# Optimization experiments

Measured on AMD Instinct MI355X. Metric: run time of the kernel, lower is better.

The kernel has to match this reference:

```python
import jax, jax.numpy as jnp
import numpy as np

B, Q, K = 8, 128, 1024
QK_DIM = 512   # query_size == key_size
HID = 256      # hidden_size
VDIM = 512     # value feature dim
NEG = -1e6     # mask fill value used by the torch code


def setup_inputs() -> dict:
    key = jax.random.key(0)
    ks = jax.random.split(key, 7)
    queries = jax.random.normal(ks[0], (B, Q, QK_DIM), dtype=jnp.float32)
    keys = jax.random.normal(ks[1], (B, K, QK_DIM), dtype=jnp.float32)
    values = jax.random.normal(ks[2], (B, K, VDIM), dtype=jnp.float32)
    valid_lens = jax.random.randint(ks[3], (B,), 1, K + 1, dtype=jnp.int32)
    # Linear weights (no bias); scaled like torch default init
    Wq = jax.random.normal(ks[4], (QK_DIM, HID), dtype=jnp.float32) / np.sqrt(QK_DIM)
    Wk = jax.random.normal(ks[5], (QK_DIM, HID), dtype=jnp.float32) / np.sqrt(QK_DIM)
    wv = jax.random.normal(ks[6], (HID,), dtype=jnp.float32) / np.sqrt(HID)
    return {"queries": queries, "keys": keys, "values": values,
            "valid_lens": valid_lens, "Wq": Wq, "Wk": Wk, "wv": wv}


def reference(queries, keys, values, valid_lens, Wq, Wk, wv):
    q = jnp.einsum('bqd,dh->bqh', queries, Wq)          # [B,Q,H]
    k = jnp.einsum('bkd,dh->bkh', keys, Wk)             # [B,K,H]
    # broadcast add -> tanh -> score projection
    features = jnp.tanh(q[:, :, None, :] + k[:, None, :, :])  # [B,Q,K,H]
    scores = jnp.einsum('bqkh,h->bqk', features, wv)    # [B,Q,K]
    # masked softmax over last axis (valid_lens per batch row)
    mask = jnp.arange(scores.shape[-1])[None, None, :] < valid_lens[:, None, None]
    scores = jnp.where(mask, scores, NEG)
    attn = jax.nn.softmax(scores, axis=-1)              # [B,Q,K]
    # dropout is identity in eval mode (p=0)
    return jnp.einsum('bqk,bkv->bqv', attn, values)     # [B,Q,VDIM]
```

## Files before the change

### kernel.cpp

```cpp
#include <hip/hip_runtime.h>
#include <math.h>

#define NB 8
#define NQ 128
#define NK 1024
#define ND 512
#define NH 256
#define NV 512

typedef __attribute__((ext_vector_type(8))) short short8v;
typedef __attribute__((ext_vector_type(4))) float floatx4;

__device__ __forceinline__ ushort f2bf(float f) {
  union { float f; unsigned u; } v; v.f = f;
  unsigned r = (v.u + 0x7FFF + ((v.u >> 16) & 1)) >> 16;
  return (ushort)r;
}
__device__ __forceinline__ float bf2f(ushort b) {
  union { unsigned u; float f; } v; v.u = ((unsigned)b) << 16;
  return v.f;
}
__device__ __forceinline__ float wave_rsum(float v) {
#pragma unroll
  for (int off = 32; off; off >>= 1) v += __shfl_xor(v, off);
  return v;
}

__global__ __launch_bounds__(256) void splitw_kernel(
    const float* __restrict__ Wq, const float* __restrict__ Wk,
    ushort* __restrict__ WtQh, ushort* __restrict__ WtQl,
    ushort* __restrict__ WtKh, ushort* __restrict__ WtKl) {
  const int t = threadIdx.x;
  const int mat = blockIdx.x >> 7;
  const int bi = blockIdx.x & 127;
  const int d0 = (bi >> 3) * 32, h0 = (bi & 7) * 32;
  const float* W = mat ? Wk : Wq;
  ushort* Oh = mat ? WtKh : WtQh;
  ushort* Ol = mat ? WtKl : WtQl;
  __shared__ float tile[32][33];
#pragma unroll
  for (int i = 0; i < 4; ++i) {
    int idx = t + 256 * i;
    int r = idx >> 5, c = idx & 31;
    tile[r][c] = W[(size_t)(d0 + r) * NH + h0 + c];
  }
  __syncthreads();
#pragma unroll
  for (int i = 0; i < 4; ++i) {
    int idx = t + 256 * i;
    int hh = idx >> 5, dd = idx & 31;
    float f = tile[dd][hh];
    ushort hi = f2bf(f);
    float lo = f - bf2f(hi);
    Oh[(size_t)(h0 + hh) * ND + d0 + dd] = hi;
    Ol[(size_t)(h0 + hh) * ND + d0 + dd] = f2bf(lo);
  }
}

__global__ __launch_bounds__(256) void convert_v_kernel(
    const float* __restrict__ values, const int* __restrict__ valid_lens,
    ushort* __restrict__ VhT) {
  const int b = blockIdx.z;
  const int k0 = blockIdx.x * 32;
  const int v0 = blockIdx.y * 32;
  const int V = valid_lens[b];
  if (k0 >= ((V + 31) & ~31)) return;
  const int t = threadIdx.x;
  __shared__ float tile[32][33];
#pragma unroll
  for (int i = 0; i < 4; ++i) {
    int idx = t + 256 * i;
    int kk = idx >> 5, vv = idx & 31;
    tile[kk][vv] = values[(size_t)(b * NK + k0 + kk) * NV + v0 + vv];
  }
  __syncthreads();
#pragma unroll
  for (int i = 0; i < 4; ++i) {
    int idx = t + 256 * i;
    int vv = idx >> 5, kk = idx & 31;
    VhT[(size_t)(b * NV + v0 + vv) * NK + k0 + kk] = f2bf(tile[kk][vv]);
  }
}

__global__ __launch_bounds__(256) void proj_mfma_kernel(
    const float* __restrict__ queries, const float* __restrict__ keys,
    const ushort* __restrict__ WtQh, const ushort* __restrict__ WtQl,
    const ushort* __restrict__ WtKh, const ushort* __restrict__ WtKl,
    const int* __restrict__ valid_lens,
    float* __restrict__ Eq, ushort* __restrict__ EkTb) {
  const int t = threadIdx.x;
  const int lane = t & 63, wvid = t >> 6;
  const int lr = lane & 15, lg = lane >> 4;
  const int bx = blockIdx.x;
  const bool isQ = bx < 64;
  const float* A;
  const ushort *Wh, *Wl;
  int arow0, b = 0, rin = 0;
  if (isQ) {
    A = queries; Wh = WtQh; Wl = WtQl; arow0 = bx * 16;
  } else {
    int kt = bx - 64;
    b = kt >> 6; rin = (kt & 63) * 16;
    if (rin >= valid_lens[b]) return;
    A = keys; Wh = WtKh; Wl = WtKl; arow0 = b * NK + rin;
  }

  __shared__ ushort Ah[16][520];
  __shared__ ushort Al[16][520];
  {
    const float* Arow = A + (size_t)arow0 * ND;
#pragma unroll
    for (int i = 0; i < 8; ++i) {
      int e = (t + 256 * i) * 4;
      int r = e >> 9, c = e & 511;
      float4 a = *(const float4*)&Arow[e];
      ushort4 h, l;
      h.x = f2bf(a.x); l.x = f2bf(a.x - bf2f(h.x));
      h.y = f2bf(a.y); l.y = f2bf(a.y - bf2f(h.y));
      h.z = f2bf(a.z); l.z = f2bf(a.z - bf2f(h.z));
      h.w = f2bf(a.w); l.w = f2bf(a.w - bf2f(h.w));
      *(ushort4*)&Ah[r][c] = h;
      *(ushort4*)&Al[r][c] = l;
    }
  }
  __syncthreads();

  const int c0w = wvid * 64;
  const ushort* Whb = Wh + (size_t)(c0w + lr) * ND + lg * 8;
  const ushort* Wlb = Wl + (size_t)(c0w + lr) * ND + lg * 8;

  floatx4 acc[4];
#pragma unroll
  for (int cf = 0; cf < 4; ++cf) acc[cf] = (floatx4){0.f, 0.f, 0.f, 0.f};

#define LOADW(dsth, dstl, kkv)                                            \
  {                                                                       \
    const size_t _d = (size_t)(kkv) * 32;                                 \
    dsth##0 = *(const short8v*)&Whb[_d];                                  \
    dstl##0 = *(const short8v*)&Wlb[_d];                                  \
    dsth##1 = *(const short8v*)&Whb[(size_t)16 * ND + _d];                \
    dstl##1 = *(const short8v*)&Wlb[(size_t)16 * ND + _d];                \
    dsth##2 = *(const short8v*)&Whb[(size_t)32 * ND + _d];                \
    dstl##2 = *(const short8v*)&Wlb[(size_t)32 * ND + _d];                \
    dsth##3 = *(const short8v*)&Whb[(size_t)48 * ND + _d];                \
    dstl##3 = *(const short8v*)&Wlb[(size_t)48 * ND + _d];                \
  }

#define MFMA4(ah_, al_, wh, wl)                                           \
  {                                                                       \
    acc[0] = __builtin_amdgcn_mfma_f32_16x16x32_bf16(al_, wh##0, acc[0], 0, 0, 0); \
    acc[0] = __builtin_amdgcn_mfma_f32_16x16x32_bf16(ah_, wl##0, acc[0], 0, 0, 0); \
    acc[0] = __builtin_amdgcn_mfma_f32_16x16x32_bf16(ah_, wh##0, acc[0], 0, 0, 0); \
    acc[1] = __builtin_amdgcn_mfma_f32_16x16x32_bf16(al_, wh##1, acc[1], 0, 0, 0); \
    acc[1] = __builtin_amdgcn_mfma_f32_16x16x32_bf16(ah_, wl##1, acc[1], 0, 0, 0); \
    acc[1] = __builtin_amdgcn_mfma_f32_16x16x32_bf16(ah_, wh##1, acc[1], 0, 0, 0); \
    acc[2] = __builtin_amdgcn_mfma_f32_16x16x32_bf16(al_, wh##2, acc[2], 0, 0, 0); \
    acc[2] = __builtin_amdgcn_mfma_f32_16x16x32_bf16(ah_, wl##2, acc[2], 0, 0, 0); \
    acc[2] = __builtin_amdgcn_mfma_f32_16x16x32_bf16(ah_, wh##2, acc[2], 0, 0, 0); \
    acc[3] = __builtin_amdgcn_mfma_f32_16x16x32_bf16(al_, wh##3, acc[3], 0, 0, 0); \
    acc[3] = __builtin_amdgcn_mfma_f32_16x16x32_bf16(ah_, wl##3, acc[3], 0, 0, 0); \
    acc[3] = __builtin_amdgcn_mfma_f32_16x16x32_bf16(ah_, wh##3, acc[3], 0, 0, 0); \
  }

  short8v wAh0, wAh1, wAh2, wAh3, wAl0, wAl1, wAl2, wAl3;
  short8v wBh0, wBh1, wBh2, wBh3, wBl0, wBl1, wBl2, wBl3;
  LOADW(wAh, wAl, 0);
#pragma unroll 1
  for (int kk = 0; kk < 16; kk += 2) {
    LOADW(wBh, wBl, kk + 1);
    {
      short8v ah_ = *(const short8v*)&Ah[lr][kk * 32 + lg * 8];
      short8v al_ = *(const short8v*)&Al[lr][kk * 32 + lg * 8];
      MFMA4(ah_, al_, wAh, wAl);
    }
    if (kk + 2 < 16) LOADW(wAh, wAl, kk + 2);
    {
      short8v ah_ = *(const short8v*)&Ah[lr][(kk + 1) * 32 + lg * 8];
      short8v al_ = *(const short8v*)&Al[lr][(kk + 1) * 32 + lg * 8];
      MFMA4(ah_, al_, wBh, wBl);
    }
  }
#undef LOADW
#undef MFMA4

  const float C2 = 2.885390081777927f;
  if (isQ) {
#pragma unroll
    for (int cf = 0; cf < 4; ++cf) {
      const int h = c0w + cf * 16 + lr;
#pragma unroll
      for (int reg = 0; reg < 4; ++reg) {
        const int row = arow0 + lg * 4 + reg;
        float p = fminf(fmaxf(acc[cf][reg], -15.f), 15.f);
        Eq[(size_t)row * NH + h] = exp2f(p * C2);
      }
    }
  } else {
#pragma unroll
    for (int cf = 0; cf < 4; ++cf) {
      const int h = c0w + cf * 16 + lr;
      ushort4 e;
      e.x = f2bf(exp2f(fminf(fmaxf(acc[cf][0], -15.f), 15.f) * C2));
      e.y = f2bf(exp2f(fminf(fmaxf(acc[cf][1], -15.f), 15.f) * C2));
      e.z = f2bf(exp2f(fminf(fmaxf(acc[cf][2], -15.f), 15.f) * C2));
      e.w = f2bf(exp2f(fminf(fmaxf(acc[cf][3], -15.f), 15.f) * C2));
      *(ushort4*)&EkTb[((size_t)(b * NH + h)) * NK + rin + lg * 4] = e;
    }
  }
}

__global__ __launch_bounds__(256) void score_kernel(
    const float* __restrict__ Eq, const ushort* __restrict__ EkTb,
    const float* __restrict__ wvp, const int* __restrict__ valid_lens,
    ushort* __restrict__ Pb, float* __restrict__ rowsum) {
  const int b = blockIdx.z;
  const int V = valid_lens[b];
  const int k0 = blockIdx.y * 256;
  if (k0 >= V) return;
  const int t = threadIdx.x;
  const int q0 = blockIdx.x * 2;
  const int lane = t & 63, wid = t >> 6;
  const float L2E2 = 2.8853900817779268f;

  __shared__ __align__(16) float eqs[2][NH];
  __shared__ __align__(16) float wvs[NH];
  __shared__ float red[8];

  if (t < 128)
    ((float4*)eqs)[t] = ((const float4*)&Eq[(size_t)(b * NQ + q0) * NH])[t];
  wvs[t] = wvp[t];
  __syncthreads();

  float mn = wave_rsum(fminf(wvs[t], 0.f));
  if (lane == 0) red[wid] = mn;
  __syncthreads();
  const float SN = -(red[0] + red[1] + red[2] + red[3]);
  __syncthreads();

  const ushort* ek = EkTb + (size_t)b * NH * NK + k0 + t;
  float acc0 = 0.f, acc1 = 0.f;

  ushort uA[8], uB[8];
#define LOADE(u, h0)                                                      \
  {                                                                       \
    _Pragma("unroll") for (int j = 0; j < 8; ++j)                         \
        u[j] = ek[(size_t)((h0) + j) * NK];                               \
  }
#define CHUNK(u, h0)                                                      \
  {                                                                       \
    float e0[8], e1[8], w8[8];                                            \
    *(float4*)&e0[0] = *(const float4*)&eqs[0][(h0)];                     \
    *(float4*)&e0[4] = *(const float4*)&eqs[0][(h0) + 4];                 \
    *(float4*)&e1[0] = *(const float4*)&eqs[1][(h0)];                     \
    *(float4*)&e1[4] = *(const float4*)&eqs[1][(h0) + 4];                 \
    *(float4*)&w8[0] = *(const float4*)&wvs[(h0)];                        \
    *(float4*)&w8[4] = *(const float4*)&wvs[(h0) + 4];                    \
    _Pragma("unroll") for (int j = 0; j < 8; ++j) {                       \
      const float ev = bf2f(u[j]);                                        \
      acc0 += w8[j] * __builtin_amdgcn_rcpf(__builtin_fmaf(e0[j], ev, 1.f)); \
      acc1 += w8[j] * __builtin_amdgcn_rcpf(__builtin_fmaf(e1[j], ev, 1.f)); \
    }                                                                     \
  }

  LOADE(uA, 0);
#pragma unroll 1
  for (int h0 = 0; h0 < NH; h0 += 16) {
    LOADE(uB, h0 + 8);
    CHUNK(uA, h0);
    if (h0 + 16 < NH) LOADE(uA, h0 + 16);
    CHUNK(uB, h0 + 8);
  }
#undef LOADE
#undef CHUNK

  const int k = k0 + t;
  const float p0 = (k < V) ? exp2f(-L2E2 * (acc0 + SN)) : 0.f;
  const float p1 = (k < V) ? exp2f(-L2E2 * (acc1 + SN)) : 0.f;
  const ushort u0 = f2bf(p0), u1 = f2bf(p1);
  Pb[(size_t)(b * NQ + q0) * NK + k] = u0;
  Pb[(size_t)(b * NQ + q0 + 1) * NK + k] = u1;

  float s0 = wave_rsum(bf2f(u0));
  float s1 = wave_rsum(bf2f(u1));
  if (lane == 0) { red[wid] = s0; red[4 + wid] = s1; }
  __syncthreads();
  if (t == 0) {
    atomicAdd(&rowsum[b * NQ + q0], red[0] + red[1] + red[2] + red[3]);
    atomicAdd(&rowsum[b * NQ + q0 + 1], red[4] + red[5] + red[6] + red[7]);
  }
}

__global__ __launch_bounds__(128) void pv_mfma_kernel(
    const ushort* __restrict__ Pb, const ushort* __restrict__ VhT,
    const float* __restrict__ rowsum, const int* __restrict__ valid_lens,
    float* __restrict__ out) {
  const int w = threadIdx.x >> 6;
  const int lane = threadIdx.x & 63;
  const int lr = lane & 15, lg = lane >> 4;
  const int qt = blockIdx.x, vt = blockIdx.y, b = blockIdx.z;
  const int V = valid_lens[b];
  const int Kt = (V + 31) >> 5;
  const int q0 = qt * 16;
  const int v0 = vt * 32 + w * 16;
  const ushort* pp = Pb + (size_t)(b * NQ + q0 + lr) * NK + lg * 8;
  const ushort* vp = VhT + (size_t)(b * NV + v0 + lr) * NK + lg * 8;

  floatx4 accA = (floatx4){0.f, 0.f, 0.f, 0.f};
  floatx4 accB = (floatx4){0.f, 0.f, 0.f, 0.f};
  short8v pa, va, pb, vb;

  pa = *(const short8v*)&pp[0];
  va = *(const short8v*)&vp[0];
  if (Kt > 1) {
    pb = *(const short8v*)&pp[32];
    vb = *(const short8v*)&vp[32];
  }
  int s = 0;
  while (s + 2 <= Kt) {
    accA = __builtin_amdgcn_mfma_f32_16x16x32_bf16(pa, va, accA, 0, 0, 0);
    if (s + 2 < Kt) {
      pa = *(const short8v*)&pp[(size_t)(s + 2) * 32];
      va = *(const short8v*)&vp[(size_t)(s + 2) * 32];
    }
    accB = __builtin_amdgcn_mfma_f32_16x16x32_bf16(pb, vb, accB, 0, 0, 0);
    if (s + 3 < Kt) {
      pb = *(const short8v*)&pp[(size_t)(s + 3) * 32];
      vb = *(const short8v*)&vp[(size_t)(s + 3) * 32];
    }
    s += 2;
  }
  if (s < Kt)
    accA = __builtin_amdgcn_mfma_f32_16x16x32_bf16(pa, va, accA, 0, 0, 0);

#pragma unroll
  for (int reg = 0; reg < 4; ++reg) {
    const int row = b * NQ + q0 + lg * 4 + reg;
    const float rs = __builtin_amdgcn_rcpf(rowsum[row]);
    out[(size_t)row * NV + v0 + lr] = (accA[reg] + accB[reg]) * rs;
  }
}

extern "C" void kernel_launch(void* const* d_in, const int* in_sizes, int n_in,
                              void* d_out, int out_size, void* d_ws, size_t ws_size,
                              hipStream_t stream) {
  const float* queries = (const float*)d_in[0];
  const float* keys    = (const float*)d_in[1];
  const float* values  = (const float*)d_in[2];
  const int*   vlens   = (const int*)d_in[3];
  const float* Wq      = (const float*)d_in[4];
  const float* Wk      = (const float*)d_in[5];
  const float* wv      = (const float*)d_in[6];
  float* out = (float*)d_out;

  char* base = (char*)d_ws;
  ushort* WtQh = (ushort*)base;
  ushort* WtQl = WtQh + NH * ND;
  ushort* WtKh = WtQl + NH * ND;
  ushort* WtKl = WtKh + NH * ND;
  float*  Eq   = (float*)(base + (1 << 20));
  ushort* EkTb = (ushort*)(base + (2 << 20));
  ushort* Pb   = (ushort*)(base + (6 << 20));
  ushort* VhT  = (ushort*)(base + (8 << 20));
  float*  rowsum = (float*)(base + (16 << 20));

  hipMemsetAsync(rowsum, 0, NB * NQ * sizeof(float), stream);
  splitw_kernel<<<dim3(256), dim3(256), 0, stream>>>(Wq, Wk, WtQh, WtQl, WtKh, WtKl);
  convert_v_kernel<<<dim3(32, 16, 8), dim3(256), 0, stream>>>(values, vlens, VhT);
  proj_mfma_kernel<<<dim3(576), dim3(256), 0, stream>>>(
      queries, keys, WtQh, WtQl, WtKh, WtKl, vlens, Eq, EkTb);
  score_kernel<<<dim3(64, 4, 8), dim3(256), 0, stream>>>(
      Eq, EkTb, wv, vlens, Pb, rowsum);
  pv_mfma_kernel<<<dim3(8, 16, 8), dim3(128), 0, stream>>>(
      Pb, VhT, rowsum, vlens, out);
}
```

Baseline: 181.4 us.

## Pack W, V and P into MFMA fragment-order tiles for contiguous lane loads

The weight split, V conversion and score kernels now write their bf16 outputs in a tiled layout that matches the MFMA operand fragments. Each lane can then load a contiguous 16-byte chunk with a lane*8 stride instead of doing strided row gathers. The projection and PV kernels are rewritten to read these packed tiles, with deeper register prefetch (triple-buffered W, four-stage P/V) and launch-bounds occupancy hints. PV now rounds the K-tile count up to a multiple of 4. That can read V tiles the conversion kernel never wrote, so any non-finite leftovers in the workspace could reach the output.

```diff
diff --git a/kernel.cpp b/kernel.cpp
--- a/kernel.cpp
+++ b/kernel.cpp
@@ -11,6 +11,7 @@
 typedef __attribute__((ext_vector_type(8))) short short8v;
 typedef __attribute__((ext_vector_type(4))) float floatx4;
 
+
 __device__ __forceinline__ ushort f2bf(float f) {
   union { float f; unsigned u; } v; v.f = f;
   unsigned r = (v.u + 0x7FFF + ((v.u >> 16) & 1)) >> 16;
@@ -26,40 +27,33 @@
   return v;
 }
 
-__global__ __launch_bounds__(256) void splitw_kernel(
+__global__ __launch_bounds__(64) void splitw_kernel(
     const float* __restrict__ Wq, const float* __restrict__ Wk,
-    ushort* __restrict__ WtQh, ushort* __restrict__ WtQl,
-    ushort* __restrict__ WtKh, ushort* __restrict__ WtKl) {
-  const int t = threadIdx.x;
-  const int mat = blockIdx.x >> 7;
-  const int bi = blockIdx.x & 127;
-  const int d0 = (bi >> 3) * 32, h0 = (bi & 7) * 32;
-  const float* W = mat ? Wk : Wq;
-  ushort* Oh = mat ? WtKh : WtQh;
-  ushort* Ol = mat ? WtKl : WtQl;
-  __shared__ float tile[32][33];
-#pragma unroll
-  for (int i = 0; i < 4; ++i) {
-    int idx = t + 256 * i;
-    int r = idx >> 5, c = idx & 31;
-    tile[r][c] = W[(size_t)(d0 + r) * NH + h0 + c];
-  }
-  __syncthreads();
-#pragma unroll
-  for (int i = 0; i < 4; ++i) {
-    int idx = t + 256 * i;
-    int hh = idx >> 5, dd = idx & 31;
-    float f = tile[dd][hh];
+    ushort* __restrict__ WpQ, ushort* __restrict__ WpK) {
+  const int l = threadIdx.x;
+  const int blk = blockIdx.x;
+  const float* W = blockIdx.y ? Wk : Wq;
+  ushort* O = blockIdx.y ? WpK : WpQ;
+  const int col = ((blk >> 4) << 4) + (l & 15);
+  const int dbase = (blk & 15) * 32 + ((l >> 4) << 3);
+  ushort h8[8], l8[8];
+#pragma unroll
+  for (int j = 0; j < 8; ++j) {
+    float f = W[(size_t)(dbase + j) * NH + col];
     ushort hi = f2bf(f);
-    float lo = f - bf2f(hi);
-    Oh[(size_t)(h0 + hh) * ND + d0 + dd] = hi;
-    Ol[(size_t)(h0 + hh) * ND + d0 + dd] = f2bf(lo);
-  }
+    h8[j] = hi;
+    l8[j] = f2bf(f - bf2f(hi));
+  }
+  ushort* oh = &O[(size_t)blk * 1024 + l * 8];
+  *(ushort4*)&oh[0] = make_ushort4(h8[0], h8[1], h8[2], h8[3]);
+  *(ushort4*)&oh[4] = make_ushort4(h8[4], h8[5], h8[6], h8[7]);
+  *(ushort4*)&oh[512] = make_ushort4(l8[0], l8[1], l8[2], l8[3]);
+  *(ushort4*)&oh[516] = make_ushort4(l8[4], l8[5], l8[6], l8[7]);
 }
 
 __global__ __launch_bounds__(256) void convert_v_kernel(
     const float* __restrict__ values, const int* __restrict__ valid_lens,
-    ushort* __restrict__ VhT) {
+    ushort* __restrict__ Vp) {
   const int b = blockIdx.z;
   const int k0 = blockIdx.x * 32;
   const int v0 = blockIdx.y * 32;
@@ -74,18 +68,21 @@
     tile[kk][vv] = values[(size_t)(b * NK + k0 + kk) * NV + v0 + vv];
   }
   __syncthreads();
-#pragma unroll
-  for (int i = 0; i < 4; ++i) {
-    int idx = t + 256 * i;
-    int vv = idx >> 5, kk = idx & 31;
-    VhT[(size_t)(b * NV + v0 + vv) * NK + k0 + kk] = f2bf(tile[kk][vv]);
-  }
-}
-
-__global__ __launch_bounds__(256) void proj_mfma_kernel(
+  const int vv = t & 31, k4 = t >> 5;
+  const int kr = k4 * 4;
+  const size_t base = ((size_t)(b * 32 + ((v0 + vv) >> 4)) * 32 + (k0 >> 5)) * 512;
+  const int off = ((vv & 15) << 3) + (((kr >> 3) & 3) << 7) + (kr & 7);
+  ushort4 o;
+  o.x = f2bf(tile[kr + 0][vv]);
+  o.y = f2bf(tile[kr + 1][vv]);
+  o.z = f2bf(tile[kr + 2][vv]);
+  o.w = f2bf(tile[kr + 3][vv]);
+  *(ushort4*)&Vp[base + off] = o;
+}
+
+__global__ __launch_bounds__(256, 2) void proj_mfma_kernel(
     const float* __restrict__ queries, const float* __restrict__ keys,
-    const ushort* __restrict__ WtQh, const ushort* __restrict__ WtQl,
-    const ushort* __restrict__ WtKh, const ushort* __restrict__ WtKl,
+    const ushort* __restrict__ WpQ, const ushort* __restrict__ WpK,
     const int* __restrict__ valid_lens,
     float* __restrict__ Eq, ushort* __restrict__ EkTb) {
   const int t = threadIdx.x;
@@ -94,15 +91,15 @@
   const int bx = blockIdx.x;
   const bool isQ = bx < 64;
   const float* A;
-  const ushort *Wh, *Wl;
+  const ushort* Wp;
   int arow0, b = 0, rin = 0;
   if (isQ) {
-    A = queries; Wh = WtQh; Wl = WtQl; arow0 = bx * 16;
+    A = queries; Wp = WpQ; arow0 = bx * 16;
   } else {
     int kt = bx - 64;
     b = kt >> 6; rin = (kt & 63) * 16;
     if (rin >= valid_lens[b]) return;
-    A = keys; Wh = WtKh; Wl = WtKl; arow0 = b * NK + rin;
+    A = keys; Wp = WpK; arow0 = b * NK + rin;
   }
 
   __shared__ ushort Ah[16][520];
@@ -125,94 +122,78 @@
   }
   __syncthreads();
 
-  const int c0w = wvid * 64;
-  const ushort* Whb = Wh + (size_t)(c0w + lr) * ND + lg * 8;
-  const ushort* Wlb = Wl + (size_t)(c0w + lr) * ND + lg * 8;
+  const ushort* wbase = Wp + (size_t)wvid * 64 * 1024 + lane * 8;
 
   floatx4 acc[4];
 #pragma unroll
-  for (int cf = 0; cf < 4; ++cf) acc[cf] = (floatx4){0.f, 0.f, 0.f, 0.f};
-
-#define LOADW(dsth, dstl, kkv)                                            \
-  {                                                                       \
-    const size_t _d = (size_t)(kkv) * 32;                                 \
-    dsth##0 = *(const short8v*)&Whb[_d];                                  \
-    dstl##0 = *(const short8v*)&Wlb[_d];                                  \
-    dsth##1 = *(const short8v*)&Whb[(size_t)16 * ND + _d];                \
-    dstl##1 = *(const short8v*)&Wlb[(size_t)16 * ND + _d];                \
-    dsth##2 = *(const short8v*)&Whb[(size_t)32 * ND + _d];                \
-    dstl##2 = *(const short8v*)&Wlb[(size_t)32 * ND + _d];                \
-    dsth##3 = *(const short8v*)&Whb[(size_t)48 * ND + _d];                \
-    dstl##3 = *(const short8v*)&Wlb[(size_t)48 * ND + _d];                \
-  }
-
-#define MFMA4(ah_, al_, wh, wl)                                           \
-  {                                                                       \
-    acc[0] = __builtin_amdgcn_mfma_f32_16x16x32_bf16(al_, wh##0, acc[0], 0, 0, 0); \
-    acc[0] = __builtin_amdgcn_mfma_f32_16x16x32_bf16(ah_, wl##0, acc[0], 0, 0, 0); \
-    acc[0] = __builtin_amdgcn_mfma_f32_16x16x32_bf16(ah_, wh##0, acc[0], 0, 0, 0); \
-    acc[1] = __builtin_amdgcn_mfma_f32_16x16x32_bf16(al_, wh##1, acc[1], 0, 0, 0); \
-    acc[1] = __builtin_amdgcn_mfma_f32_16x16x32_bf16(ah_, wl##1, acc[1], 0, 0, 0); \
-    acc[1] = __builtin_amdgcn_mfma_f32_16x16x32_bf16(ah_, wh##1, acc[1], 0, 0, 0); \
-    acc[2] = __builtin_amdgcn_mfma_f32_16x16x32_bf16(al_, wh##2, acc[2], 0, 0, 0); \
-    acc[2] = __builtin_amdgcn_mfma_f32_16x16x32_bf16(ah_, wl##2, acc[2], 0, 0, 0); \
-    acc[2] = __builtin_amdgcn_mfma_f32_16x16x32_bf16(ah_, wh##2, acc[2], 0, 0, 0); \
-    acc[3] = __builtin_amdgcn_mfma_f32_16x16x32_bf16(al_, wh##3, acc[3], 0, 0, 0); \
-    acc[3] = __builtin_amdgcn_mfma_f32_16x16x32_bf16(ah_, wl##3, acc[3], 0, 0, 0); \
-    acc[3] = __builtin_amdgcn_mfma_f32_16x16x32_bf16(ah_, wh##3, acc[3], 0, 0, 0); \
-  }
-
-  short8v wAh0, wAh1, wAh2, wAh3, wAl0, wAl1, wAl2, wAl3;
-  short8v wBh0, wBh1, wBh2, wBh3, wBl0, wBl1, wBl2, wBl3;
-  LOADW(wAh, wAl, 0);
-#pragma unroll 1
-  for (int kk = 0; kk < 16; kk += 2) {
-    LOADW(wBh, wBl, kk + 1);
-    {
-      short8v ah_ = *(const short8v*)&Ah[lr][kk * 32 + lg * 8];
-      short8v al_ = *(const short8v*)&Al[lr][kk * 32 + lg * 8];
-      MFMA4(ah_, al_, wAh, wAl);
+  for (int c = 0; c < 4; ++c) acc[c] = (floatx4){0.f, 0.f, 0.f, 0.f};
+
+  short8v wh[3][4], wl[3][4];
+  short8v ahb[2], alb[2];
+
+#define LOADW(buf, kkv)                                                    \
+  {                                                                        \
+    _Pragma("unroll") for (int c = 0; c < 4; ++c) {                        \
+      wh[buf][c] = *(const short8v*)&wbase[(size_t)(c * 16 + (kkv)) * 1024];        \
+      wl[buf][c] = *(const short8v*)&wbase[(size_t)(c * 16 + (kkv)) * 1024 + 512];  \
+    }                                                                      \
+  }
+#define LOADA(buf, kkv)                                                    \
+  {                                                                        \
+    ahb[buf] = *(const short8v*)&Ah[lr][(kkv) * 32 + lg * 8];              \
+    alb[buf] = *(const short8v*)&Al[lr][(kkv) * 32 + lg * 8];              \
+  }
+
+  LOADW(0, 0);
+  LOADW(1, 1);
+  LOADA(0, 0);
+#pragma unroll
+  for (int kk = 0; kk < 16; ++kk) {
+    if (kk + 2 < 16) LOADW((kk + 2) % 3, kk + 2);
+    if (kk + 1 < 16) LOADA((kk + 1) & 1, kk + 1);
+    const short8v ah_ = ahb[kk & 1];
+    const short8v al_ = alb[kk & 1];
+    const int B = kk % 3;
+#pragma unroll
+    for (int c = 0; c < 4; ++c) {
+      acc[c] = __builtin_amdgcn_mfma_f32_16x16x32_bf16(al_, wh[B][c], acc[c], 0, 0, 0);
+      acc[c] = __builtin_amdgcn_mfma_f32_16x16x32_bf16(ah_, wl[B][c], acc[c], 0, 0, 0);
+      acc[c] = __builtin_amdgcn_mfma_f32_16x16x32_bf16(ah_, wh[B][c], acc[c], 0, 0, 0);
     }
-    if (kk + 2 < 16) LOADW(wAh, wAl, kk + 2);
-    {
-      short8v ah_ = *(const short8v*)&Ah[lr][(kk + 1) * 32 + lg * 8];
-      short8v al_ = *(const short8v*)&Al[lr][(kk + 1) * 32 + lg * 8];
-      MFMA4(ah_, al_, wBh, wBl);
-    }
   }
 #undef LOADW
-#undef MFMA4
+#undef LOADA
 
   const float C2 = 2.885390081777927f;
   if (isQ) {
 #pragma unroll
-    for (int cf = 0; cf < 4; ++cf) {
-      const int h = c0w + cf * 16 + lr;
+    for (int c = 0; c < 4; ++c) {
+      const int h = wvid * 64 + c * 16 + lr;
 #pragma unroll
       for (int reg = 0; reg < 4; ++reg) {
         const int row = arow0 + lg * 4 + reg;
-        float p = fminf(fmaxf(acc[cf][reg], -15.f), 15.f);
+        float p = fminf(fmaxf(acc[c][reg], -15.f), 15.f);
         Eq[(size_t)row * NH + h] = exp2f(p * C2);
       }
     }
   } else {
 #pragma unroll
-    for (int cf = 0; cf < 4; ++cf) {
-      const int h = c0w + cf * 16 + lr;
+    for (int c = 0; c < 4; ++c) {
+      const int h = wvid * 64 + c * 16 + lr;
       ushort4 e;
-      e.x = f2bf(exp2f(fminf(fmaxf(acc[cf][0], -15.f), 15.f) * C2));
-      e.y = f2bf(exp2f(fminf(fmaxf(acc[cf][1], -15.f), 15.f) * C2));
-      e.z = f2bf(exp2f(fminf(fmaxf(acc[cf][2], -15.f), 15.f) * C2));
-      e.w = f2bf(exp2f(fminf(fmaxf(acc[cf][3], -15.f), 15.f) * C2));
+      e.x = f2bf(exp2f(fminf(fmaxf(acc[c][0], -15.f), 15.f) * C2));
+      e.y = f2bf(exp2f(fminf(fmaxf(acc[c][1], -15.f), 15.f) * C2));
+      e.z = f2bf(exp2f(fminf(fmaxf(acc[c][2], -15.f), 15.f) * C2));
+      e.w = f2bf(exp2f(fminf(fmaxf(acc[c][3], -15.f), 15.f) * C2));
       *(ushort4*)&EkTb[((size_t)(b * NH + h)) * NK + rin + lg * 4] = e;
     }
   }
 }
 
-__global__ __launch_bounds__(256) void score_kernel(
+__global__ __launch_bounds__(256, 2) void score_kernel(
     const float* __restrict__ Eq, const ushort* __restrict__ EkTb,
     const float* __restrict__ wvp, const int* __restrict__ valid_lens,
-    ushort* __restrict__ Pb, float* __restrict__ rowsum) {
+    ushort* __restrict__ Pbp, float* __restrict__ rowsum) {
   const int b = blockIdx.z;
   const int V = valid_lens[b];
   const int k0 = blockIdx.y * 256;
@@ -277,8 +258,13 @@
   const float p0 = (k < V) ? exp2f(-L2E2 * (acc0 + SN)) : 0.f;
   const float p1 = (k < V) ? exp2f(-L2E2 * (acc1 + SN)) : 0.f;
   const ushort u0 = f2bf(p0), u1 = f2bf(p1);
-  Pb[(size_t)(b * NQ + q0) * NK + k] = u0;
-  Pb[(size_t)(b * NQ + q0 + 1) * NK + k] = u1;
+
+  {
+    const size_t blk0 = ((size_t)(b * 8 + (q0 >> 4)) * 32 + (k0 >> 5) + (t >> 5)) * 512;
+    const int offk = (((t >> 3) & 3) << 7) + (t & 7);
+    Pbp[blk0 + ((q0 & 15) << 3) + offk] = u0;
+    Pbp[blk0 + (((q0 + 1) & 15) << 3) + offk] = u1;
+  }
 
   float s0 = wave_rsum(bf2f(u0));
   float s1 = wave_rsum(bf2f(u1));
@@ -290,53 +276,47 @@
   }
 }
 
-__global__ __launch_bounds__(128) void pv_mfma_kernel(
-    const ushort* __restrict__ Pb, const ushort* __restrict__ VhT,
+__global__ __launch_bounds__(128, 2) void pv_mfma_kernel(
+    const ushort* __restrict__ Pbp, const ushort* __restrict__ Vp,
     const float* __restrict__ rowsum, const int* __restrict__ valid_lens,
     float* __restrict__ out) {
   const int w = threadIdx.x >> 6;
   const int lane = threadIdx.x & 63;
   const int lr = lane & 15, lg = lane >> 4;
-  const int qt = blockIdx.x, vt = blockIdx.y, b = blockIdx.z;
+  const int qt = blockIdx.x, vt2 = blockIdx.y, b = blockIdx.z;
   const int V = valid_lens[b];
-  const int Kt = (V + 31) >> 5;
-  const int q0 = qt * 16;
-  const int v0 = vt * 32 + w * 16;
-  const ushort* pp = Pb + (size_t)(b * NQ + q0 + lr) * NK + lg * 8;
-  const ushort* vp = VhT + (size_t)(b * NV + v0 + lr) * NK + lg * 8;
-
-  floatx4 accA = (floatx4){0.f, 0.f, 0.f, 0.f};
-  floatx4 accB = (floatx4){0.f, 0.f, 0.f, 0.f};
-  short8v pa, va, pb, vb;
-
-  pa = *(const short8v*)&pp[0];
-  va = *(const short8v*)&vp[0];
-  if (Kt > 1) {
-    pb = *(const short8v*)&pp[32];
-    vb = *(const short8v*)&vp[32];
-  }
-  int s = 0;
-  while (s + 2 <= Kt) {
-    accA = __builtin_amdgcn_mfma_f32_16x16x32_bf16(pa, va, accA, 0, 0, 0);
-    if (s + 2 < Kt) {
-      pa = *(const short8v*)&pp[(size_t)(s + 2) * 32];
-      va = *(const short8v*)&vp[(size_t)(s + 2) * 32];
-    }
-    accB = __builtin_amdgcn_mfma_f32_16x16x32_bf16(pb, vb, accB, 0, 0, 0);
-    if (s + 3 < Kt) {
-      pb = *(const short8v*)&pp[(size_t)(s + 3) * 32];
-      vb = *(const short8v*)&vp[(size_t)(s + 3) * 32];
-    }
-    s += 2;
-  }
-  if (s < Kt)
-    accA = __builtin_amdgcn_mfma_f32_16x16x32_bf16(pa, va, accA, 0, 0, 0);
+  const int Kt4 = (((V + 31) >> 5) + 3) & ~3;
+  const int vt = vt2 * 2 + w;
+  const ushort* pbase = Pbp + ((size_t)(b * 8 + qt) * 32) * 512 + lane * 8;
+  const ushort* vbase = Vp + ((size_t)(b * 32 + vt) * 32) * 512 + lane * 8;
+
+#define LP(s) (*(const short8v*)&pbase[(size_t)(s) * 512])
+#define LV(s) (*(const short8v*)&vbase[(size_t)(s) * 512])
+
+  floatx4 acc0 = (floatx4){0.f, 0.f, 0.f, 0.f};
+  floatx4 acc1 = (floatx4){0.f, 0.f, 0.f, 0.f};
+  short8v pA, vA, pB, vB, pC, vC, pD, vD;
+  pA = LP(0); vA = LV(0);
+  pB = LP(1); vB = LV(1);
+  pC = LP(2); vC = LV(2);
+  for (int s = 0; s < Kt4; s += 4) {
+    pD = LP(s + 3); vD = LV(s + 3);
+    acc0 = __builtin_amdgcn_mfma_f32_16x16x32_bf16(pA, vA, acc0, 0, 0, 0);
+    if (s + 4 < Kt4) { pA = LP(s + 4); vA = LV(s + 4); }
+    acc1 = __builtin_amdgcn_mfma_f32_16x16x32_bf16(pB, vB, acc1, 0, 0, 0);
+    if (s + 5 < Kt4) { pB = LP(s + 5); vB = LV(s + 5); }
+    acc0 = __builtin_amdgcn_mfma_f32_16x16x32_bf16(pC, vC, acc0, 0, 0, 0);
+    if (s + 6 < Kt4) { pC = LP(s + 6); vC = LV(s + 6); }
+    acc1 = __builtin_amdgcn_mfma_f32_16x16x32_bf16(pD, vD, acc1, 0, 0, 0);
+  }
+#undef LP
+#undef LV
 
 #pragma unroll
   for (int reg = 0; reg < 4; ++reg) {
-    const int row = b * NQ + q0 + lg * 4 + reg;
+    const int row = b * NQ + qt * 16 + lg * 4 + reg;
     const float rs = __builtin_amdgcn_rcpf(rowsum[row]);
-    out[(size_t)row * NV + v0 + lr] = (accA[reg] + accB[reg]) * rs;
+    out[(size_t)row * NV + vt * 16 + lr] = (acc0[reg] + acc1[reg]) * rs;
   }
 }
 
@@ -353,23 +333,21 @@
   float* out = (float*)d_out;
 
   char* base = (char*)d_ws;
-  ushort* WtQh = (ushort*)base;
-  ushort* WtQl = WtQh + NH * ND;
-  ushort* WtKh = WtQl + NH * ND;
-  ushort* WtKl = WtKh + NH * ND;
+  ushort* WpQ  = (ushort*)base;
+  ushort* WpK  = WpQ + 256 * 1024;
   float*  Eq   = (float*)(base + (1 << 20));
   ushort* EkTb = (ushort*)(base + (2 << 20));
-  ushort* Pb   = (ushort*)(base + (6 << 20));
-  ushort* VhT  = (ushort*)(base + (8 << 20));
+  ushort* Pbp  = (ushort*)(base + (6 << 20));
+  ushort* Vp   = (ushort*)(base + (8 << 20));
   float*  rowsum = (float*)(base + (16 << 20));
 
   hipMemsetAsync(rowsum, 0, NB * NQ * sizeof(float), stream);
-  splitw_kernel<<<dim3(256), dim3(256), 0, stream>>>(Wq, Wk, WtQh, WtQl, WtKh, WtKl);
-  convert_v_kernel<<<dim3(32, 16, 8), dim3(256), 0, stream>>>(values, vlens, VhT);
+  splitw_kernel<<<dim3(256, 2), dim3(64), 0, stream>>>(Wq, Wk, WpQ, WpK);
+  convert_v_kernel<<<dim3(32, 16, 8), dim3(256), 0, stream>>>(values, vlens, Vp);
   proj_mfma_kernel<<<dim3(576), dim3(256), 0, stream>>>(
-      queries, keys, WtQh, WtQl, WtKh, WtKl, vlens, Eq, EkTb);
+      queries, keys, WpQ, WpK, vlens, Eq, EkTb);
   score_kernel<<<dim3(64, 4, 8), dim3(256), 0, stream>>>(
-      Eq, EkTb, wv, vlens, Pb, rowsum);
+      Eq, EkTb, wv, vlens, Pbp, rowsum);
   pv_mfma_kernel<<<dim3(8, 16, 8), dim3(128), 0, stream>>>(
-      Pb, VhT, rowsum, vlens, out);
-}
+      Pbp, Vp, rowsum, vlens, out);
+}
```

Result: faster. 153.8 us (-15.2%).
